# Optimization experiments

Hardware: AMD Instinct MI355X
Metric: run time of the kernel (lower is better)

Reference implementation:

```python
import jax, jax.numpy as jnp
import numpy as np

# 47 skeleton edges (parent, child) from getSkeletalModelStructure()
EDGES = np.array([
    (0, 1), (1, 2), (2, 3), (3, 29), (1, 5), (5, 6), (6, 8), (8, 9), (8, 13),
    (8, 17), (8, 21), (8, 25), (9, 10), (10, 11), (11, 12), (13, 14), (14, 15),
    (15, 16), (17, 18), (18, 19), (19, 20), (21, 22), (22, 23), (23, 24),
    (25, 26), (26, 27), (27, 28), (29, 30), (29, 34), (29, 38), (29, 42),
    (29, 46), (30, 31), (31, 32), (32, 33), (34, 35), (35, 36), (36, 37),
    (38, 39), (39, 40), (40, 41), (42, 43), (43, 44), (44, 45), (46, 47),
    (47, 48), (48, 49)], dtype=np.int32)

N_JOINTS = 50
N_EDGES = 47


def _length_direct(pose):
    # pose: [B, T, 151]; drop counter channel, view as joints
    B, T = pose.shape[0], pose.shape[1]
    p = pose[..., :-1].reshape(B, T, N_JOINTS, 3)
    diff = p[:, :, EDGES[:, 0], :] - p[:, :, EDGES[:, 1], :]   # [B, T, 47, 3]
    length = jnp.linalg.norm(diff, axis=-1)                      # [B, T, 47]
    eps = jnp.finfo(pose.dtype).tiny
    direct = diff / (length + eps)[..., None]                    # [B, T, 47, 3]
    # torch stacks each [B,T,3] edge dir along dim=-1 -> [B,T,3,47], then reshapes
    directs = jnp.transpose(direct, (0, 1, 3, 2)).reshape(B, T, N_EDGES * 3)
    return length, directs


def setup_inputs() -> dict:
    key = jax.random.key(0)
    k1, k2 = jax.random.split(key)
    B, T, D = 128, 1024, 151
    preds = jax.random.normal(k1, (B, T, D), dtype=jnp.float32)
    targets = jax.random.normal(k2, (B, T, D), dtype=jnp.float32)
    return {"preds": preds, "targets": targets}


def reference(preds, targets):
    target_pad = 0.0
    mask = (targets != target_pad).astype(preds.dtype)           # [B, T, 151]
    preds_m = preds * mask
    targets_m = targets * mask
    _, preds_dir = _length_direct(preds_m)
    _, targets_dir = _length_direct(targets_m)
    preds_dir = preds_dir * mask[:, :, :N_EDGES * 3]
    targets_dir = targets_dir * mask[:, :, :N_EDGES * 3]
    # cfg: loss='l1' (mean abs), vel_loss='mse' (mean square), loss_scale=1.0
    l1 = jnp.mean(jnp.abs(preds_m - targets_m))
    vel_mse = jnp.mean(jnp.square(preds_dir - targets_dir))
    return l1 + 0.1 * vel_mse
```

## Files before the change

kernel.cpp:

```cpp
#include <hip/hip_runtime.h>


#define N_ROWS   (128 * 1024)
#define ROW      151
#define N_EDGES  47
#define GRID     1024
#define BLOCK    256
#define FP_SCALE 1048576.0

__constant__ int c_par[N_EDGES] = {
    0, 1, 2, 3, 1, 5, 6, 8, 8, 8, 8, 8, 9, 10, 11, 13, 14, 15, 17, 18, 19,
    21, 22, 23, 25, 26, 27, 29, 29, 29, 29, 29, 30, 31, 32, 34, 35, 36, 38,
    39, 40, 42, 43, 44, 46, 47, 48};
__constant__ int c_chd[N_EDGES] = {
    1, 2, 3, 29, 5, 6, 8, 9, 13, 17, 21, 25, 10, 11, 12, 14, 15, 16, 18, 19,
    20, 22, 23, 24, 26, 27, 28, 30, 34, 38, 42, 46, 31, 32, 33, 35, 36, 37,
    39, 40, 41, 43, 44, 45, 47, 48, 49};

__global__ __launch_bounds__(BLOCK) void reg_loss_main(
        const float* __restrict__ preds, const float* __restrict__ targets,
        unsigned long long* __restrict__ ws) {
    __shared__ float pmS[4][152];
    __shared__ float tmS[4][152];
    __shared__ float redL[4], redV[4];

    const int lane = threadIdx.x & 63;
    const int wave = threadIdx.x >> 6;

    int pi = 0, ci = 0;
    if (lane < N_EDGES) {
        pi = c_par[lane] * 3;
        ci = c_chd[lane] * 3;
    }

    float l1 = 0.f;
    float vel = 0.f;

    const int waveGlobal = blockIdx.x * 4 + wave;
    const int waveStride = GRID * 4;

    for (int row = waveGlobal; row < N_ROWS; row += waveStride) {
        const long long base = (long long)row * ROW;
#pragma unroll
        for (int k = 0; k < 3; ++k) {
            int idx = lane + k * 64;
            if (idx < ROW) {
                float t = targets[base + idx];
                float p = preds[base + idx];
                float pm = (t != 0.f) ? p : 0.f;
                l1 += fabsf(pm - t);
                pmS[wave][idx] = pm;
                tmS[wave][idx] = t;
            }
        }
        __syncthreads();
        if (lane < N_EDGES) {
            float pdx = pmS[wave][pi]     - pmS[wave][ci];
            float pdy = pmS[wave][pi + 1] - pmS[wave][ci + 1];
            float pdz = pmS[wave][pi + 2] - pmS[wave][ci + 2];
            float tdx = tmS[wave][pi]     - tmS[wave][ci];
            float tdy = tmS[wave][pi + 1] - tmS[wave][ci + 1];
            float tdz = tmS[wave][pi + 2] - tmS[wave][ci + 2];
            const float eps = 1.17549435e-38f;
            float plen = sqrtf(pdx * pdx + pdy * pdy + pdz * pdz);
            float tlen = sqrtf(tdx * tdx + tdy * tdy + tdz * tdz);
            float pinv = 1.f / (plen + eps);
            float tinv = 1.f / (tlen + eps);
            float dx = pdx * pinv - tdx * tinv;
            float dy = pdy * pinv - tdy * tinv;
            float dz = pdz * pinv - tdz * tinv;
            float m0 = (tmS[wave][lane]          != 0.f) ? 1.f : 0.f;
            float m1 = (tmS[wave][47 + lane]     != 0.f) ? 1.f : 0.f;
            float m2 = (tmS[wave][94 + lane]     != 0.f) ? 1.f : 0.f;
            vel += m0 * dx * dx + m1 * dy * dy + m2 * dz * dz;
        }
        __syncthreads();
    }

#pragma unroll
    for (int off = 32; off > 0; off >>= 1) {
        l1  += __shfl_down(l1, off);
        vel += __shfl_down(vel, off);
    }
    if (lane == 0) { redL[wave] = l1; redV[wave] = vel; }
    __syncthreads();
    if (threadIdx.x == 0) {
        float L = redL[0] + redL[1] + redL[2] + redL[3];
        float V = redV[0] + redV[1] + redV[2] + redV[3];
        unsigned long long uL = (unsigned long long)((double)L * FP_SCALE + 0.5);
        unsigned long long uV = (unsigned long long)((double)V * FP_SCALE + 0.5);
        atomicAdd(&ws[0], uL);
        atomicAdd(&ws[1], uV);
    }
}

__global__ void reg_loss_finalize(const unsigned long long* __restrict__ ws,
                                  float* __restrict__ out) {
    if (threadIdx.x == 0 && blockIdx.x == 0) {
        double L = (double)ws[0] * (1.0 / FP_SCALE);
        double V = (double)ws[1] * (1.0 / FP_SCALE);
        double res = L / ((double)N_ROWS * 151.0)
                   + 0.1 * (V / ((double)N_ROWS * 141.0));
        out[0] = (float)res;
    }
}

extern "C" void kernel_launch(void* const* d_in, const int* in_sizes, int n_in,
                              void* d_out, int out_size, void* d_ws, size_t ws_size,
                              hipStream_t stream) {
    const float* preds   = (const float*)d_in[0];
    const float* targets = (const float*)d_in[1];
    unsigned long long* ws = (unsigned long long*)d_ws;
    float* out = (float*)d_out;

    hipMemsetAsync(d_ws, 0, 2 * sizeof(unsigned long long), stream);
    reg_loss_main<<<GRID, BLOCK, 0, stream>>>(preds, targets, ws);
    reg_loss_finalize<<<1, 64, 0, stream>>>(ws, out);
}
```

Measured before the change: 199.4 us.

## Tile 16 rows per block with float4 loads and per-block partial sums

Each block now stages 16-row tiles (16*151 floats, divisible by 4) into shared memory using coalesced float4 loads, then spreads the 16*47 edge tasks across all 256 threads instead of idling lanes 47-63 of each wave. The grid doubles to 2048 blocks with four tiles each, giving exact coverage without a grid-stride loop. The fixed-point atomics and the memset are replaced by per-block partial sums written to the workspace and reduced in double precision by a 256-thread finalize kernel. The tiling removes scalar per-row loads and halves the barriers per row, at the cost of integer divisions to map each element to its row and column and more shared memory per block.

```diff
diff --git a/kernel.cpp b/kernel.cpp
--- a/kernel.cpp
+++ b/kernel.cpp
@@ -4,77 +4,102 @@
 #define N_ROWS   (128 * 1024)
 #define ROW      151
 #define N_EDGES  47
-#define GRID     1024
+#define GRID     2048
 #define BLOCK    256
-#define FP_SCALE 1048576.0
+#define TILE_ROWS 16
+#define TILES_PER_BLOCK 4
+#define TILE_DWORDS (TILE_ROWS * ROW)
+#define TILE_F4 (TILE_DWORDS / 4)
+#define N_TASKS (TILE_ROWS * N_EDGES)
 
-__constant__ int c_par[N_EDGES] = {
-    0, 1, 2, 3, 1, 5, 6, 8, 8, 8, 8, 8, 9, 10, 11, 13, 14, 15, 17, 18, 19,
-    21, 22, 23, 25, 26, 27, 29, 29, 29, 29, 29, 30, 31, 32, 34, 35, 36, 38,
-    39, 40, 42, 43, 44, 46, 47, 48};
-__constant__ int c_chd[N_EDGES] = {
-    1, 2, 3, 29, 5, 6, 8, 9, 13, 17, 21, 25, 10, 11, 12, 14, 15, 16, 18, 19,
-    20, 22, 23, 24, 26, 27, 28, 30, 34, 38, 42, 46, 31, 32, 33, 35, 36, 37,
-    39, 40, 41, 43, 44, 45, 47, 48, 49};
+__constant__ unsigned int c_edge[N_EDGES] = {
+    (0*3)|(1*3<<16),  (1*3)|(2*3<<16),  (2*3)|(3*3<<16),  (3*3)|(29*3<<16),
+    (1*3)|(5*3<<16),  (5*3)|(6*3<<16),  (6*3)|(8*3<<16),  (8*3)|(9*3<<16),
+    (8*3)|(13*3<<16), (8*3)|(17*3<<16), (8*3)|(21*3<<16), (8*3)|(25*3<<16),
+    (9*3)|(10*3<<16), (10*3)|(11*3<<16),(11*3)|(12*3<<16),(13*3)|(14*3<<16),
+    (14*3)|(15*3<<16),(15*3)|(16*3<<16),(17*3)|(18*3<<16),(18*3)|(19*3<<16),
+    (19*3)|(20*3<<16),(21*3)|(22*3<<16),(22*3)|(23*3<<16),(23*3)|(24*3<<16),
+    (25*3)|(26*3<<16),(26*3)|(27*3<<16),(27*3)|(28*3<<16),(29*3)|(30*3<<16),
+    (29*3)|(34*3<<16),(29*3)|(38*3<<16),(29*3)|(42*3<<16),(29*3)|(46*3<<16),
+    (30*3)|(31*3<<16),(31*3)|(32*3<<16),(32*3)|(33*3<<16),(34*3)|(35*3<<16),
+    (35*3)|(36*3<<16),(36*3)|(37*3<<16),(38*3)|(39*3<<16),(39*3)|(40*3<<16),
+    (40*3)|(41*3<<16),(42*3)|(43*3<<16),(43*3)|(44*3<<16),(44*3)|(45*3<<16),
+    (46*3)|(47*3<<16),(47*3)|(48*3<<16),(48*3)|(49*3<<16)};
 
 __global__ __launch_bounds__(BLOCK) void reg_loss_main(
         const float* __restrict__ preds, const float* __restrict__ targets,
-        unsigned long long* __restrict__ ws) {
-    __shared__ float pmS[4][152];
-    __shared__ float tmS[4][152];
+        float* __restrict__ wsL, float* __restrict__ wsV) {
+    __shared__ float pmS[TILE_ROWS][ROW + 1];
+    __shared__ float tmS[TILE_ROWS][ROW + 1];
     __shared__ float redL[4], redV[4];
 
-    const int lane = threadIdx.x & 63;
-    const int wave = threadIdx.x >> 6;
-
-    int pi = 0, ci = 0;
-    if (lane < N_EDGES) {
-        pi = c_par[lane] * 3;
-        ci = c_chd[lane] * 3;
-    }
+    const int t = threadIdx.x;
+    const int lane = t & 63;
+    const int wave = t >> 6;
 
     float l1 = 0.f;
     float vel = 0.f;
 
-    const int waveGlobal = blockIdx.x * 4 + wave;
-    const int waveStride = GRID * 4;
+    for (int tile = 0; tile < TILES_PER_BLOCK; ++tile) {
+        const long long tileIdx = (long long)blockIdx.x * TILES_PER_BLOCK + tile;
+        const float4* __restrict__ p4 =
+            (const float4*)(preds + tileIdx * TILE_DWORDS);
+        const float4* __restrict__ t4 =
+            (const float4*)(targets + tileIdx * TILE_DWORDS);
 
-    for (int row = waveGlobal; row < N_ROWS; row += waveStride) {
-        const long long base = (long long)row * ROW;
+        if (tile) __syncthreads();
+
 #pragma unroll
         for (int k = 0; k < 3; ++k) {
-            int idx = lane + k * 64;
-            if (idx < ROW) {
-                float t = targets[base + idx];
-                float p = preds[base + idx];
-                float pm = (t != 0.f) ? p : 0.f;
-                l1 += fabsf(pm - t);
-                pmS[wave][idx] = pm;
-                tmS[wave][idx] = t;
+            int i = t + k * BLOCK;
+            if (i < TILE_F4) {
+                float4 pv = p4[i];
+                float4 tv = t4[i];
+                float pe[4] = {pv.x, pv.y, pv.z, pv.w};
+                float te[4] = {tv.x, tv.y, tv.z, tv.w};
+                int d0 = i * 4;
+#pragma unroll
+                for (int j = 0; j < 4; ++j) {
+                    int d = d0 + j;
+                    int r = d / ROW;
+                    int c = d - r * ROW;
+                    float tt = te[j];
+                    float pm = (tt != 0.f) ? pe[j] : 0.f;
+                    l1 += fabsf(pm - tt);
+                    pmS[r][c] = pm;
+                    tmS[r][c] = tt;
+                }
             }
         }
         __syncthreads();
-        if (lane < N_EDGES) {
-            float pdx = pmS[wave][pi]     - pmS[wave][ci];
-            float pdy = pmS[wave][pi + 1] - pmS[wave][ci + 1];
-            float pdz = pmS[wave][pi + 2] - pmS[wave][ci + 2];
-            float tdx = tmS[wave][pi]     - tmS[wave][ci];
-            float tdy = tmS[wave][pi + 1] - tmS[wave][ci + 1];
-            float tdz = tmS[wave][pi + 2] - tmS[wave][ci + 2];
-            const float eps = 1.17549435e-38f;
-            float plen = sqrtf(pdx * pdx + pdy * pdy + pdz * pdz);
-            float tlen = sqrtf(tdx * tdx + tdy * tdy + tdz * tdz);
-            float pinv = 1.f / (plen + eps);
-            float tinv = 1.f / (tlen + eps);
-            float dx = pdx * pinv - tdx * tinv;
-            float dy = pdy * pinv - tdy * tinv;
-            float dz = pdz * pinv - tdz * tinv;
-            float m0 = (tmS[wave][lane]          != 0.f) ? 1.f : 0.f;
-            float m1 = (tmS[wave][47 + lane]     != 0.f) ? 1.f : 0.f;
-            float m2 = (tmS[wave][94 + lane]     != 0.f) ? 1.f : 0.f;
-            vel += m0 * dx * dx + m1 * dy * dy + m2 * dz * dz;
+
+#pragma unroll
+        for (int k = 0; k < 3; ++k) {
+            int task = t + k * BLOCK;
+            if (task < N_TASKS) {
+                int r = task / N_EDGES;
+                int e = task - r * N_EDGES;
+                unsigned int pk = c_edge[e];
+                int pi = pk & 0xffff;
+                int ci = pk >> 16;
+                float pdx = pmS[r][pi]     - pmS[r][ci];
+                float pdy = pmS[r][pi + 1] - pmS[r][ci + 1];
+                float pdz = pmS[r][pi + 2] - pmS[r][ci + 2];
+                float tdx = tmS[r][pi]     - tmS[r][ci];
+                float tdy = tmS[r][pi + 1] - tmS[r][ci + 1];
+                float tdz = tmS[r][pi + 2] - tmS[r][ci + 2];
+                const float eps = 1.17549435e-38f;
+                float pinv = 1.f / (sqrtf(pdx*pdx + pdy*pdy + pdz*pdz) + eps);
+                float tinv = 1.f / (sqrtf(tdx*tdx + tdy*tdy + tdz*tdz) + eps);
+                float dx = pdx * pinv - tdx * tinv;
+                float dy = pdy * pinv - tdy * tinv;
+                float dz = pdz * pinv - tdz * tinv;
+                float m0 = (tmS[r][e]      != 0.f) ? 1.f : 0.f;
+                float m1 = (tmS[r][47 + e] != 0.f) ? 1.f : 0.f;
+                float m2 = (tmS[r][94 + e] != 0.f) ? 1.f : 0.f;
+                vel += m0 * dx * dx + m1 * dy * dy + m2 * dz * dz;
+            }
         }
-        __syncthreads();
     }
 
 #pragma unroll
@@ -84,24 +109,33 @@
     }
     if (lane == 0) { redL[wave] = l1; redV[wave] = vel; }
     __syncthreads();
-    if (threadIdx.x == 0) {
-        float L = redL[0] + redL[1] + redL[2] + redL[3];
-        float V = redV[0] + redV[1] + redV[2] + redV[3];
-        unsigned long long uL = (unsigned long long)((double)L * FP_SCALE + 0.5);
-        unsigned long long uV = (unsigned long long)((double)V * FP_SCALE + 0.5);
-        atomicAdd(&ws[0], uL);
-        atomicAdd(&ws[1], uV);
+    if (t == 0) {
+        wsL[blockIdx.x] = redL[0] + redL[1] + redL[2] + redL[3];
+        wsV[blockIdx.x] = redV[0] + redV[1] + redV[2] + redV[3];
     }
 }
 
-__global__ void reg_loss_finalize(const unsigned long long* __restrict__ ws,
-                                  float* __restrict__ out) {
-    if (threadIdx.x == 0 && blockIdx.x == 0) {
-        double L = (double)ws[0] * (1.0 / FP_SCALE);
-        double V = (double)ws[1] * (1.0 / FP_SCALE);
-        double res = L / ((double)N_ROWS * 151.0)
-                   + 0.1 * (V / ((double)N_ROWS * 141.0));
-        out[0] = (float)res;
+__global__ __launch_bounds__(BLOCK) void reg_loss_finalize(
+        const float* __restrict__ wsL, const float* __restrict__ wsV,
+        float* __restrict__ out) {
+    __shared__ double rl[4], rv[4];
+    const int t = threadIdx.x;
+    const int lane = t & 63;
+    const int wave = t >> 6;
+    double L = 0.0, V = 0.0;
+    for (int k = t; k < GRID; k += BLOCK) { L += wsL[k]; V += wsV[k]; }
+#pragma unroll
+    for (int off = 32; off > 0; off >>= 1) {
+        L += __shfl_down(L, off);
+        V += __shfl_down(V, off);
+    }
+    if (lane == 0) { rl[wave] = L; rv[wave] = V; }
+    __syncthreads();
+    if (t == 0) {
+        double Ls = rl[0] + rl[1] + rl[2] + rl[3];
+        double Vs = rv[0] + rv[1] + rv[2] + rv[3];
+        out[0] = (float)(Ls / ((double)N_ROWS * 151.0)
+                       + 0.1 * (Vs / ((double)N_ROWS * 141.0)));
     }
 }
 
@@ -110,10 +144,10 @@
                               hipStream_t stream) {
     const float* preds   = (const float*)d_in[0];
     const float* targets = (const float*)d_in[1];
-    unsigned long long* ws = (unsigned long long*)d_ws;
+    float* wsL = (float*)d_ws;
+    float* wsV = wsL + GRID;
     float* out = (float*)d_out;
 
-    hipMemsetAsync(d_ws, 0, 2 * sizeof(unsigned long long), stream);
-    reg_loss_main<<<GRID, BLOCK, 0, stream>>>(preds, targets, ws);
-    reg_loss_finalize<<<1, 64, 0, stream>>>(ws, out);
+    reg_loss_main<<<GRID, BLOCK, 0, stream>>>(preds, targets, wsL, wsV);
+    reg_loss_finalize<<<1, BLOCK, 0, stream>>>(wsL, wsV, out);
 }
```

New measurement: 189.2 us. -5.1%, faster.
